# Performance work log

Hardware: AMD Instinct MI355X
Metric: run time of the kernel (lower is better)

Reference implementation:

```python
import jax, jax.numpy as jnp
import numpy as np

N = 4096       # graph nodes (= image batch)
FIN = 2048     # resnet50 feature dim
HD = 256       # hidden_dim
C = 10         # num_classes
THRESH = 0.05  # cosine-sim threshold for adjacency
ATTN_SLOPE = 0.2   # DGL GATConv leaky-relu slope
MLP_SLOPE = 0.01   # F.leaky_relu default slope


def setup_inputs() -> dict:
    key = jax.random.key(0)
    ks = jax.random.split(key, 24)
    g = lambda k, shp, s=0.05: (jax.random.normal(k, shp, jnp.float32) * s)
    inp = {
        "x": jax.random.normal(ks[0], (N, FIN), jnp.float32),
        # GAT layer 1: 2048 -> 256, 4 heads, linear residual
        "W0": g(ks[1], (FIN, 4 * HD)),
        "al0": g(ks[2], (4, HD)), "ar0": g(ks[3], (4, HD)),
        "b0": jnp.zeros((4 * HD,), jnp.float32),
        "R0": g(ks[4], (FIN, 4 * HD)),
        # GAT mid layer: 256 -> 256, 4 heads, linear residual
        "W1": g(ks[5], (HD, 4 * HD)),
        "al1": g(ks[6], (4, HD)), "ar1": g(ks[7], (4, HD)),
        "b1": jnp.zeros((4 * HD,), jnp.float32),
        "R1": g(ks[8], (HD, 4 * HD)),
        # GAT final layer: 256 -> 256, 1 head, identity residual
        "W2": g(ks[9], (HD, HD)),
        "al2": g(ks[10], (1, HD)), "ar2": g(ks[11], (1, HD)),
        "b2": jnp.zeros((HD,), jnp.float32),
        # heads
        "Wl1": g(ks[12], (FIN + HD, 1024)), "bl1": jnp.zeros((1024,), jnp.float32),
        "Wc1": g(ks[13], (1024, C)), "bc1": jnp.zeros((C,), jnp.float32),
        "Wc2": g(ks[14], (FIN, C)), "bc2": jnp.zeros((C,), jnp.float32),
    }
    return inp


def _gat(h, mask, W, al, ar, b, R):
    """DGL GATConv with residual=True, masked dense edge-softmax.
    h: [N, Fin]; mask: [N, N] bool (mask[dst, src]); returns [N, H, Fout]."""
    n = h.shape[0]
    H, F = al.shape
    feat = (h @ W).reshape(n, H, F)                      # [N, H, F] src/dst projections
    el = jnp.einsum('nhf,hf->nh', feat, al)              # src score
    er = jnp.einsum('nhf,hf->nh', feat, ar)              # dst score
    e = er[:, None, :] + el[None, :, :]                  # [dst, src, H]
    e = jnp.where(e > 0, e, ATTN_SLOPE * e)              # leaky relu
    e = jnp.where(mask[:, :, None], e, -jnp.inf)
    alpha = jax.nn.softmax(e, axis=1)                    # edge softmax over src
    rst = jnp.einsum('dsh,shf->dhf', alpha, feat)        # aggregate
    res = (h @ R).reshape(n, H, F) if R is not None else h.reshape(n, -1, F)
    return rst + res + b.reshape(1, H, F)


def reference(x, W0, al0, ar0, b0, R0, W1, al1, ar1, b1, R1,
              W2, al2, ar2, b2, Wl1, bl1, Wc1, bc1, Wc2, bc2):
    # dynamic threshold graph from cosine similarity
    xn = x / jnp.linalg.norm(x, axis=1, keepdims=True)
    mask = (xn @ xn.T) > THRESH                          # symmetric, includes self-loops
    # stacked GAT layers, heads summed
    h = jax.nn.relu(_gat(x, mask, W0, al0, ar0, b0, R0).sum(axis=1))
    h = jax.nn.relu(_gat(h, mask, W1, al1, ar1, b1, R1).sum(axis=1))
    h = _gat(h, mask, W2, al2, ar2, b2, None).sum(axis=1)  # last layer: no relu
    # MLP heads
    z = jnp.concatenate([x, h], axis=1)                  # [N, 2048+256]
    z = jax.nn.leaky_relu(z @ Wl1 + bl1, MLP_SLOPE)
    logits_1 = z @ Wc1 + bc1
    logits_2 = x @ Wc2 + bc2
    return logits_1, logits_2
```

## Files before the change

kernel.cpp:

```cpp
#include <hip/hip_runtime.h>
#include <cstdint>
#include <cstddef>

#define NNODE 4096
#define FIND  2048
#define HD_   256
#define NC_   10
#define THRESH_ 0.05f
#define LOG2E_ 1.4426950408889634f

typedef unsigned long long u64;
typedef __attribute__((ext_vector_type(8))) short bf16x8;
typedef __attribute__((ext_vector_type(4))) float f32x4;

__device__ inline unsigned short f2bf_rne(float f){
  unsigned u = __builtin_bit_cast(unsigned, f);
  unsigned r = u + 0x7FFFu + ((u >> 16) & 1u);
  return (unsigned short)(r >> 16);
}
__device__ inline float bf2f(unsigned short h){
  unsigned u = ((unsigned)h) << 16;
  return __builtin_bit_cast(float, u);
}
__device__ __forceinline__ float fexp2(float x){ return __builtin_amdgcn_exp2f(x); }

__device__ __forceinline__ void gld16(const void* g, void* l){
  __builtin_amdgcn_global_load_lds(
      (const __attribute__((address_space(1))) unsigned int*)g,
      (__attribute__((address_space(3))) unsigned int*)l, 16, 0, 0);
}

__global__ void rownorm_bf(const float* __restrict__ x,
                           unsigned short* __restrict__ oh, unsigned short* __restrict__ ol){
  int row = blockIdx.x; int t = threadIdx.x;
  const float4* xr = reinterpret_cast<const float4*>(x + (size_t)row*FIND);
  float s = 0.f;
  #pragma unroll
  for (int i = 0; i < FIND/4/256; ++i){
    float4 v = xr[t + i*256];
    s += v.x*v.x + v.y*v.y + v.z*v.z + v.w*v.w;
  }
  #pragma unroll
  for (int o = 32; o > 0; o >>= 1) s += __shfl_down(s, o);
  __shared__ float red[4];
  __shared__ float invn;
  if ((t & 63) == 0) red[t >> 6] = s;
  __syncthreads();
  if (t == 0) invn = rsqrtf(red[0] + red[1] + red[2] + red[3]);
  __syncthreads();
  float inv = invn;
  #pragma unroll
  for (int i = 0; i < FIND/4/256; ++i){
    float4 v = xr[t + i*256];
    float a[4] = {v.x*inv, v.y*inv, v.z*inv, v.w*inv};
    ushort4 hv, lv;
    unsigned short* hp = &hv.x; unsigned short* lp = &lv.x;
    #pragma unroll
    for (int j = 0; j < 4; ++j){
      unsigned short h = f2bf_rne(a[j]);
      hp[j] = h; lp[j] = f2bf_rne(a[j] - bf2f(h));
    }
    size_t off = (size_t)row*FIND + (t + i*256)*4;
    *reinterpret_cast<ushort4*>(oh + off) = hv;
    *reinterpret_cast<ushort4*>(ol + off) = lv;
  }
}

__global__ void f2bf1_k(const float* __restrict__ in, unsigned short* __restrict__ oh, int n4){
  int idx = blockIdx.x*256 + threadIdx.x;
  if (idx >= n4) return;
  float4 v = reinterpret_cast<const float4*>(in)[idx];
  ushort4 hv;
  hv.x = f2bf_rne(v.x); hv.y = f2bf_rne(v.y);
  hv.z = f2bf_rne(v.z); hv.w = f2bf_rne(v.w);
  reinterpret_cast<ushort4*>(oh)[idx] = hv;
}

template<int H>
__global__ void foldT_k(const float* __restrict__ R, unsigned short* __restrict__ oh,
                        unsigned short* __restrict__ ol, int K, int F, int ktiles){
  int bid = blockIdx.x;
  int f0 = (bid / ktiles) * 64, k0 = (bid % ktiles) * 64;
  __shared__ float tile[64][65];
  int t = threadIdx.x;
  {
    int tf = t & 63, tk4 = t >> 6;
    #pragma unroll
    for (int m = 0; m < 16; ++m){
      int kl = tk4 + m*4;
      float s = 0.f;
      #pragma unroll
      for (int h = 0; h < H; ++h)
        s += R[(size_t)(k0 + kl)*(H*F) + h*F + f0 + tf];
      tile[kl][tf] = s;
    }
  }
  __syncthreads();
  {
    int tk = t & 63, tf4 = t >> 6;
    #pragma unroll
    for (int m = 0; m < 16; ++m){
      int fl = tf4 + m*4;
      float s = tile[tk][fl];
      unsigned short hv = f2bf_rne(s);
      size_t o = (size_t)(f0 + fl)*K + k0 + tk;
      oh[o] = hv;
      ol[o] = f2bf_rne(s - bf2f(hv));
    }
  }
}

__global__ void bfold_k(const float* __restrict__ b, float* __restrict__ out, int H, int F){
  int f = threadIdx.x;
  if (f < F){
    float s = 0.f;
    for (int h = 0; h < H; ++h) s += b[h*F + f];
    out[f] = s;
  }
}

__global__ void mega_gemm(const unsigned short* __restrict__ XNh, const unsigned short* __restrict__ XNl,
                          const unsigned short* __restrict__ Xh,
                          const unsigned short* __restrict__ W0h, const unsigned short* __restrict__ W0l,
                          const unsigned short* __restrict__ WLh, const unsigned short* __restrict__ WLl,
                          float* __restrict__ FT, unsigned short* __restrict__ FTB,
                          float* __restrict__ Z1, u64* __restrict__ Mk){
  __shared__ unsigned short smem[4*128*32];
  unsigned short* sAh = smem;
  unsigned short* sAl = smem + 4096;
  unsigned short* sBh = smem + 8192;
  unsigned short* sBl = smem + 12288;
  const int t = threadIdx.x, lane = t & 63, w = t >> 6;
  const int wr = w >> 1, wc = w & 1, l15 = lane & 15, lg = lane >> 4;

  const int bid = blockIdx.x;
  const int xcd = bid & 7, idx = bid >> 3;

  int role, brow, bcol;
  const unsigned short *Ah, *Al = nullptr, *Bh, *Bl;
  float* C = nullptr; int ldc = 0; size_t ldb;
  if (idx < 66){
    role = 0;
    int g = xcd*66 + idx;
    int rem = g, i = 0;
    while (rem >= 32 - i){ rem -= 32 - i; ++i; }
    brow = i; bcol = i + rem;
    Ah = XNh; Al = XNl; Bh = XNh; Bl = XNl; ldb = FIND;
  } else if (idx < 106){
    role = 1;
    int l = xcd*40 + (idx - 66);
    brow = l / 10; bcol = l % 10;
    Ah = Xh; Bh = W0h; Bl = W0l; ldb = FIND;
    C = FT; ldc = 1280;
  } else {
    role = 2;
    int l = xcd*32 + (idx - 106);
    brow = l >> 3; bcol = l & 7;
    Ah = Xh; Bh = WLh; Bl = WLl; ldb = 2304;
    C = Z1; ldc = 1024;
  }
  const bool three = (role == 0);
  const int row0 = brow*128, col0 = bcol*128;

  const int c0 = 2*w, c1 = 2*w + 1;
  const int rsub = lane >> 2, piece = lane & 3;
  const size_t ld2a = (size_t)FIND*2, ld2b = ldb*2;
  const size_t a0 = (size_t)(row0 + 16*c0 + rsub)*ld2a + piece*16;
  const size_t a1 = (size_t)(row0 + 16*c1 + rsub)*ld2a + piece*16;
  const size_t b0 = (size_t)(col0 + 16*c0 + rsub)*ld2b + piece*16;
  const size_t b1 = (size_t)(col0 + 16*c1 + rsub)*ld2b + piece*16;
  const char* pA0h = (const char*)Ah + a0;  const char* pA1h = (const char*)Ah + a1;
  const char* pA0l = three ? (const char*)Al + a0 : nullptr;
  const char* pA1l = three ? (const char*)Al + a1 : nullptr;
  const char* pB0h = (const char*)Bh + b0;  const char* pB1h = (const char*)Bh + b1;
  const char* pB0l = (const char*)Bl + b0;  const char* pB1l = (const char*)Bl + b1;
  char* lA0h = (char*)sAh + c0*1024;  char* lA1h = (char*)sAh + c1*1024;
  char* lA0l = (char*)sAl + c0*1024;  char* lA1l = (char*)sAl + c1*1024;
  char* lB0h = (char*)sBh + c0*1024;  char* lB1h = (char*)sBh + c1*1024;
  char* lB0l = (char*)sBl + c0*1024;  char* lB1l = (char*)sBl + c1*1024;

  f32x4 acc[4][4] = {};
  for (int kt = 0; kt < 64; ++kt){
    __syncthreads();
    gld16(pA0h, lA0h); gld16(pA1h, lA1h);
    if (three){
      gld16(pA0l, lA0l); gld16(pA1l, lA1l);
      pA0l += 64; pA1l += 64;
    }
    gld16(pB0h, lB0h); gld16(pB1h, lB1h);
    gld16(pB0l, lB0l); gld16(pB1l, lB1l);
    pA0h += 64; pA1h += 64;
    pB0h += 64; pB1h += 64; pB0l += 64; pB1l += 64;
    __syncthreads();
    bf16x8 fb_h[4], fb_l[4];
    #pragma unroll
    for (int j = 0; j < 4; ++j){
      int bo = (wc*64 + j*16 + l15)*32 + lg*8;
      fb_h[j] = *reinterpret_cast<const bf16x8*>(sBh + bo);
      fb_l[j] = *reinterpret_cast<const bf16x8*>(sBl + bo);
    }
    #pragma unroll
    for (int i = 0; i < 4; ++i){
      int ao = (wr*64 + i*16 + l15)*32 + lg*8;
      bf16x8 fah = *reinterpret_cast<const bf16x8*>(sAh + ao);
      #pragma unroll
      for (int j = 0; j < 4; ++j){
        acc[i][j] = __builtin_amdgcn_mfma_f32_16x16x32_bf16(fah, fb_h[j], acc[i][j], 0, 0, 0);
        acc[i][j] = __builtin_amdgcn_mfma_f32_16x16x32_bf16(fah, fb_l[j], acc[i][j], 0, 0, 0);
      }
      if (three){
        bf16x8 fal = *reinterpret_cast<const bf16x8*>(sAl + ao);
        #pragma unroll
        for (int j = 0; j < 4; ++j)
          acc[i][j] = __builtin_amdgcn_mfma_f32_16x16x32_bf16(fal, fb_h[j], acc[i][j], 0, 0, 0);
      }
    }
  }

  if (role == 0){
    #pragma unroll
    for (int i = 0; i < 4; ++i){
      #pragma unroll
      for (int r = 0; r < 4; ++r){
        u64 bits = 0ull;
        #pragma unroll
        for (int j = 0; j < 4; ++j)
          if (acc[i][j][r] > THRESH_) bits |= 1ull << (j*16 + l15);
        #pragma unroll
        for (int m = 1; m <= 8; m <<= 1) bits |= __shfl_xor(bits, m);
        if (l15 == 0){
          int gr = row0 + wr*64 + i*16 + lg*4 + r;
          Mk[(size_t)gr*64 + (col0 >> 6) + wc] = bits;
        }
      }
    }
    if (row0 != col0){
      #pragma unroll
      for (int j = 0; j < 4; ++j){
        u64 tb = 0ull;
        #pragma unroll
        for (int i = 0; i < 4; ++i)
          #pragma unroll
          for (int r = 0; r < 4; ++r)
            if (acc[i][j][r] > THRESH_) tb |= 1ull << (i*16 + lg*4 + r);
        tb |= __shfl_xor(tb, 16);
        tb |= __shfl_xor(tb, 32);
        if (lg == 0){
          int gc = col0 + wc*64 + j*16 + l15;
          Mk[(size_t)gc*64 + (row0 >> 6) + wr] = tb;
        }
      }
    }
  } else {
    const int f32min = (role == 1) ? 1024 : 0;
    #pragma unroll
    for (int i = 0; i < 4; ++i){
      int gr = row0 + wr*64 + i*16 + lg*4;
      #pragma unroll
      for (int j = 0; j < 4; ++j){
        int gc = col0 + wc*64 + j*16 + l15;
        #pragma unroll
        for (int r = 0; r < 4; ++r){
          float v = acc[i][j][r];
          if (role == 1) FTB[(size_t)(gr + r)*1280 + gc] = f2bf_rne(v);
          if (gc >= f32min) C[(size_t)(gr + r)*ldc + gc] = v;
        }
      }
    }
  }
}

template<int EPI>
__global__ void gemm_bf(const unsigned short* __restrict__ Ah,
                        const unsigned short* __restrict__ Bh, const unsigned short* __restrict__ Bl,
                        float* __restrict__ C, unsigned short* __restrict__ Cb,
                        int K, int lda, int ldb, int ldc, int gridx,
                        const float* __restrict__ bias, float param, int f32min){
  __shared__ unsigned short smem[3*128*32];
  unsigned short* sAh = smem;
  unsigned short* sBh = smem + 4096;
  unsigned short* sBl = smem + 8192;
  const int t = threadIdx.x, lane = t & 63, w = t >> 6;
  const int wr = w >> 1, wc = w & 1, l15 = lane & 15, lg = lane >> 4;

  int nwg = gridDim.x, bid = blockIdx.x;
  int wg = ((nwg & 7) == 0) ? ((bid & 7)*(nwg >> 3) + (bid >> 3)) : bid;
  int brow = wg / gridx, bcol = wg % gridx;
  const int row0 = brow*128, col0 = bcol*128;

  const int c0 = 2*w, c1 = 2*w + 1;
  const int rsub = lane >> 2, piece = lane & 3;
  const size_t ld2a = (size_t)lda*2, ld2b = (size_t)ldb*2;
  const size_t a0 = (size_t)(row0 + 16*c0 + rsub)*ld2a + piece*16;
  const size_t a1 = (size_t)(row0 + 16*c1 + rsub)*ld2a + piece*16;
  const size_t b0 = (size_t)(col0 + 16*c0 + rsub)*ld2b + piece*16;
  const size_t b1 = (size_t)(col0 + 16*c1 + rsub)*ld2b + piece*16;
  const char* pA0h = (const char*)Ah + a0;  const char* pA1h = (const char*)Ah + a1;
  const char* pB0h = (const char*)Bh + b0;  const char* pB1h = (const char*)Bh + b1;
  const char* pB0l = (const char*)Bl + b0;  const char* pB1l = (const char*)Bl + b1;
  char* lA0h = (char*)sAh + c0*1024;  char* lA1h = (char*)sAh + c1*1024;
  char* lB0h = (char*)sBh + c0*1024;  char* lB1h = (char*)sBh + c1*1024;
  char* lB0l = (char*)sBl + c0*1024;  char* lB1l = (char*)sBl + c1*1024;

  f32x4 acc[4][4] = {};
  const int nk = K >> 5;
  for (int kt = 0; kt < nk; ++kt){
    __syncthreads();
    gld16(pA0h, lA0h); gld16(pA1h, lA1h);
    gld16(pB0h, lB0h); gld16(pB1h, lB1h);
    gld16(pB0l, lB0l); gld16(pB1l, lB1l);
    pA0h += 64; pA1h += 64;
    pB0h += 64; pB1h += 64; pB0l += 64; pB1l += 64;
    __syncthreads();
    bf16x8 fb_h[4], fb_l[4];
    #pragma unroll
    for (int j = 0; j < 4; ++j){
      int bo = (wc*64 + j*16 + l15)*32 + lg*8;
      fb_h[j] = *reinterpret_cast<const bf16x8*>(sBh + bo);
      fb_l[j] = *reinterpret_cast<const bf16x8*>(sBl + bo);
    }
    #pragma unroll
    for (int i = 0; i < 4; ++i){
      int ao = (wr*64 + i*16 + l15)*32 + lg*8;
      bf16x8 fah = *reinterpret_cast<const bf16x8*>(sAh + ao);
      #pragma unroll
      for (int j = 0; j < 4; ++j){
        acc[i][j] = __builtin_amdgcn_mfma_f32_16x16x32_bf16(fah, fb_h[j], acc[i][j], 0, 0, 0);
        acc[i][j] = __builtin_amdgcn_mfma_f32_16x16x32_bf16(fah, fb_l[j], acc[i][j], 0, 0, 0);
      }
    }
  }

  #pragma unroll
  for (int i = 0; i < 4; ++i){
    int gr = row0 + wr*64 + i*16 + lg*4;
    #pragma unroll
    for (int j = 0; j < 4; ++j){
      int gc = col0 + wc*64 + j*16 + l15;
      #pragma unroll
      for (int r = 0; r < 4; ++r){
        float v = acc[i][j][r];
        size_t o = (size_t)(gr + r)*ldc + gc;
        if (EPI == 3){
          v += C[o] + bias[gc];
          v = v > 0.f ? v : param*v;
          C[o] = v;
        } else {
          if (Cb) Cb[o] = f2bf_rne(v);
          if (gc >= f32min) C[o] = v;
        }
      }
    }
  }
}

template<int H>
__global__ void el_er_k(const unsigned short* __restrict__ feat, int ldf,
                        const float* __restrict__ al, const float* __restrict__ ar,
                        float* __restrict__ el2, float* __restrict__ er2){
  int n = blockIdx.x, t = threadIdx.x;
  __shared__ float red[8];
  #pragma unroll
  for (int h = 0; h < H; ++h){
    float v = bf2f(feat[(size_t)n*ldf + h*HD_ + t]);
    float a = v * al[h*HD_ + t];
    float b = v * ar[h*HD_ + t];
    #pragma unroll
    for (int o = 32; o > 0; o >>= 1){ a += __shfl_down(a, o); b += __shfl_down(b, o); }
    if ((t & 63) == 0){ red[t >> 6] = a; red[4 + (t >> 6)] = b; }
    __syncthreads();
    if (t == 0){
      el2[n*H + h] = (red[0] + red[1] + red[2] + red[3]) * LOG2E_;
      er2[n*H + h] = (red[4] + red[5] + red[6] + red[7]) * LOG2E_;
    }
    __syncthreads();
  }
}

template<int H>
__global__ void elmax_k(const float* __restrict__ el2, float* __restrict__ out){
  int h = blockIdx.x, t = threadIdx.x;
  float m = -1e30f;
  for (int n = t; n < NNODE; n += 256) m = fmaxf(m, el2[(size_t)n*H + h]);
  #pragma unroll
  for (int o = 32; o > 0; o >>= 1) m = fmaxf(m, __shfl_down(m, o));
  __shared__ float red[4];
  if ((t & 63) == 0) red[t >> 6] = m;
  __syncthreads();
  if (t == 0) out[h] = fmaxf(fmaxf(red[0], red[1]), fmaxf(red[2], red[3]));
}

template<int H, bool RELU, bool OUTF32>
__global__ void sagg_k(const unsigned short* __restrict__ FTB, int ldf,
                       const u64* __restrict__ Mk,
                       const float* __restrict__ el2, const float* __restrict__ er2,
                       const float* __restrict__ melg2,
                       const float* __restrict__ res, int ldres,
                       const float* __restrict__ bias,
                       float* __restrict__ outf,
                       unsigned short* __restrict__ oh){
  int d = blockIdx.x, t = threadIdx.x;
  const int g = t >> 6, q = t & 63;
  const int h = (H == 4) ? g : 0;
  const int wlo = (H == 1) ? g*16 : 0;
  const int whi = (H == 1) ? wlo + 16 : 64;
  const float er2d = er2[(size_t)d*H + h];
  const float sub = er2d + melg2[h];
  const float m2 = fmaxf(sub, 0.2f*sub);
  const unsigned short* fb = FTB + 4*q + ((H == 4) ? 256*g : 0);
  float4 acc = {0.f, 0.f, 0.f, 0.f};
  float sm = 0.f;
  for (int wdi = wlo; wdi < whi; ++wdi){
    u64 bits = Mk[(size_t)d*64 + wdi];
    while (bits){
      int b = __builtin_ctzll(bits);
      bits &= bits - 1ull;
      int s = wdi*64 + b;
      float sc = er2d + el2[(size_t)s*H + h];
      sc = fmaxf(sc, 0.2f*sc);
      float wt = fexp2(sc - m2);
      sm += wt;
      ushort4 v = *reinterpret_cast<const ushort4*>(fb + (size_t)s*ldf);
      acc.x += wt*bf2f(v.x); acc.y += wt*bf2f(v.y);
      acc.z += wt*bf2f(v.z); acc.w += wt*bf2f(v.w);
    }
  }
  __shared__ float lred[4][256];
  __shared__ float lsm[4];
  if (H == 4){
    float inv = 1.f / sm;
    acc.x *= inv; acc.y *= inv; acc.z *= inv; acc.w *= inv;
  } else if (q == 0){
    lsm[g] = sm;
  }
  lred[g][q*4+0] = acc.x; lred[g][q*4+1] = acc.y;
  lred[g][q*4+2] = acc.z; lred[g][q*4+3] = acc.w;
  __syncthreads();
  float v = ((lred[0][t] + lred[1][t]) + lred[2][t]) + lred[3][t];
  if (H == 1) v /= (lsm[0] + lsm[1]) + (lsm[2] + lsm[3]);
  v += res[(size_t)d*ldres + t] + bias[t];
  if (RELU) v = fmaxf(v, 0.f);
  if (OUTF32) outf[(size_t)d*HD_ + t] = v;
  oh[(size_t)d*HD_ + t] = f2bf_rne(v);
}

__global__ void head_k(const float* __restrict__ A, int K, const float* __restrict__ W,
                       const float* __restrict__ b, float* __restrict__ out){
  int row = blockIdx.x, t = threadIdx.x;
  float p[NC_];
  #pragma unroll
  for (int j = 0; j < NC_; ++j) p[j] = 0.f;
  for (int k = t; k < K; k += 256){
    float a = A[(size_t)row*K + k];
    #pragma unroll
    for (int j = 0; j < NC_; ++j) p[j] += a * W[k*NC_ + j];
  }
  #pragma unroll
  for (int j = 0; j < NC_; ++j){
    #pragma unroll
    for (int o = 32; o > 0; o >>= 1) p[j] += __shfl_down(p[j], o);
  }
  __shared__ float red[4][NC_];
  if ((t & 63) == 0){
    #pragma unroll
    for (int j = 0; j < NC_; ++j) red[t >> 6][j] = p[j];
  }
  __syncthreads();
  if (t < NC_)
    out[(size_t)row*NC_ + t] = red[0][t] + red[1][t] + red[2][t] + red[3][t] + b[t];
}

extern "C" void kernel_launch(void* const* d_in, const int* in_sizes, int n_in,
                              void* d_out, int out_size, void* d_ws, size_t ws_size,
                              hipStream_t stream){
  const float* x   = (const float*)d_in[0];
  const float* W0  = (const float*)d_in[1];
  const float* al0 = (const float*)d_in[2];
  const float* ar0 = (const float*)d_in[3];
  const float* b0  = (const float*)d_in[4];
  const float* R0  = (const float*)d_in[5];
  const float* W1  = (const float*)d_in[6];
  const float* al1 = (const float*)d_in[7];
  const float* ar1 = (const float*)d_in[8];
  const float* b1  = (const float*)d_in[9];
  const float* R1  = (const float*)d_in[10];
  const float* W2  = (const float*)d_in[11];
  const float* al2 = (const float*)d_in[12];
  const float* ar2 = (const float*)d_in[13];
  const float* b2  = (const float*)d_in[14];
  const float* Wl1 = (const float*)d_in[15];
  const float* bl1 = (const float*)d_in[16];
  const float* Wc1 = (const float*)d_in[17];
  const float* bc1 = (const float*)d_in[18];
  const float* Wc2 = (const float*)d_in[19];
  const float* bc2 = (const float*)d_in[20];
  (void)in_sizes; (void)n_in; (void)out_size; (void)ws_size;

  char* ws = (char*)d_ws;
  size_t off = 0;
  auto alloc = [&](size_t bytes)->char*{
    char* p = ws + off; off += (bytes + 255) & ~(size_t)255; return p;
  };
  typedef unsigned short us;
  u64* MASK = (u64*)alloc((size_t)NNODE*64*8);
  us* W0h = (us*)alloc((size_t)1280*2048*2);  us* W0l = (us*)alloc((size_t)1280*2048*2);
  us* W1h = (us*)alloc((size_t)1280*256*2);   us* W1l = (us*)alloc((size_t)1280*256*2);
  us* W2h = (us*)alloc((size_t)256*256*2);    us* W2l = (us*)alloc((size_t)256*256*2);
  us* WLh = (us*)alloc((size_t)1024*2304*2);  us* WLl = (us*)alloc((size_t)1024*2304*2);
  float* BF0 = (float*)alloc(256*4);
  float* BF1 = (float*)alloc(256*4);
  float* EL2 = (float*)alloc((size_t)NNODE*4*4);
  float* ER2 = (float*)alloc((size_t)NNODE*4*4);
  float* MELG = (float*)alloc(4*4);
  us* XNh = (us*)alloc((size_t)NNODE*FIND*2);
  us* XNl = (us*)alloc((size_t)NNODE*FIND*2);
  us* Xh  = (us*)alloc((size_t)NNODE*FIND*2);
  float* FT = (float*)alloc((size_t)NNODE*1280*4);
  us* FTB = (us*)alloc((size_t)NNODE*1280*2);
  float* H2 = (float*)alloc((size_t)NNODE*HD_*4);
  us* H1h = (us*)alloc((size_t)NNODE*HD_*2);
  us* H2h = (us*)alloc((size_t)NNODE*HD_*2);
  us* H3h = (us*)alloc((size_t)NNODE*HD_*2);
  float* Z1 = (float*)alloc((size_t)NNODE*1024*4);

  float* out1 = (float*)d_out;
  float* out2 = out1 + (size_t)NNODE*NC_;

  foldT_k<1><<<512, 256, 0, stream>>>(W0, W0h, W0l, 2048, 1024, 32);
  foldT_k<4><<<128, 256, 0, stream>>>(R0, W0h + (size_t)1024*2048, W0l + (size_t)1024*2048, 2048, 256, 32);
  foldT_k<1><<< 64, 256, 0, stream>>>(W1, W1h, W1l, 256, 1024, 4);
  foldT_k<4><<< 16, 256, 0, stream>>>(R1, W1h + (size_t)1024*256, W1l + (size_t)1024*256, 256, 256, 4);
  foldT_k<1><<< 16, 256, 0, stream>>>(W2, W2h, W2l, 256, 256, 4);
  foldT_k<1><<<576, 256, 0, stream>>>(Wl1, WLh, WLl, 2304, 1024, 36);
  bfold_k<<<1, 256, 0, stream>>>(b0, BF0, 4, 256);
  bfold_k<<<1, 256, 0, stream>>>(b1, BF1, 4, 256);
  f2bf1_k<<<(NNODE*FIND/4+255)/256, 256, 0, stream>>>(x, Xh, NNODE*FIND/4);
  rownorm_bf<<<NNODE, 256, 0, stream>>>(x, XNh, XNl);

  mega_gemm<<<1104, 256, 0, stream>>>(XNh, XNl, Xh, W0h, W0l, WLh, WLl, FT, FTB, Z1, MASK);

  el_er_k<4><<<NNODE, 256, 0, stream>>>(FTB, 1280, al0, ar0, EL2, ER2);
  elmax_k<4><<<4, 256, 0, stream>>>(EL2, MELG);
  sagg_k<4,true,false><<<NNODE, 256, 0, stream>>>(FTB, 1280, MASK, EL2, ER2, MELG,
      FT + 1024, 1280, BF0, nullptr, H1h);

  gemm_bf<0><<<320, 256, 0, stream>>>(H1h, W1h, W1l, FT, FTB,
      256, 256, 256, 1280, 10, nullptr, 0.f, 1024);
  el_er_k<4><<<NNODE, 256, 0, stream>>>(FTB, 1280, al1, ar1, EL2, ER2);
  elmax_k<4><<<4, 256, 0, stream>>>(EL2, MELG);
  sagg_k<4,true,true><<<NNODE, 256, 0, stream>>>(FTB, 1280, MASK, EL2, ER2, MELG,
      FT + 1024, 1280, BF1, H2, H2h);

  gemm_bf<0><<<64, 256, 0, stream>>>(H2h, W2h, W2l, FT, FTB,
      256, 256, 256, 256, 2, nullptr, 0.f, 1 << 30);
  el_er_k<1><<<NNODE, 256, 0, stream>>>(FTB, 256, al2, ar2, EL2, ER2);
  elmax_k<1><<<1, 256, 0, stream>>>(EL2, MELG);
  sagg_k<1,false,false><<<NNODE, 256, 0, stream>>>(FTB, 256, MASK, EL2, ER2, MELG,
      H2, 256, b2, nullptr, H3h);

  gemm_bf<3><<<256, 256, 0, stream>>>(H3h, WLh + 2048, WLl + 2048, Z1, nullptr,
      256, 256, 2304, 1024, 8, bl1, 0.01f, 0);

  head_k<<<NNODE, 256, 0, stream>>>(Z1, 1024, Wc1, bc1, out1);
  head_k<<<NNODE, 256, 0, stream>>>(x, FIND, Wc2, bc2, out2);
}
```

Baseline: 536.6 us.

## Fold attention vectors into weights and fuse score computation into aggregation

Precomputes W·al and W·ar per head so the src and dst attention scores become small GEMVs on the layer input instead of reductions over projected features. Layer-0 scores are computed from x in fp32 by a new GEMV kernel, and scores for the next layer are produced in the epilogue of each aggregation kernel. The per-head max is tracked with an atomicMax on order-preserving encoded floats. This removes the separate el_er and elmax launches and drops bf16 writes of the residual columns, at the cost of extra prep kernels and atomics, with slightly different rounding since scores now come from fp32 inputs rather than bf16 features.

```diff
diff --git a/kernel.cpp b/kernel.cpp
--- a/kernel.cpp
+++ b/kernel.cpp
@@ -23,6 +23,15 @@
   return __builtin_bit_cast(float, u);
 }
 __device__ __forceinline__ float fexp2(float x){ return __builtin_amdgcn_exp2f(x); }
+
+__device__ inline unsigned fenc(float f){
+  unsigned u = __builtin_bit_cast(unsigned, f);
+  return (u & 0x80000000u) ? ~u : (u | 0x80000000u);
+}
+__device__ inline float fdec(unsigned k){
+  unsigned u = (k & 0x80000000u) ? (k & 0x7FFFFFFFu) : ~k;
+  return __builtin_bit_cast(float, u);
+}
 
 __device__ __forceinline__ void gld16(const void* g, void* l){
   __builtin_amdgcn_global_load_lds(
@@ -116,6 +125,60 @@
     float s = 0.f;
     for (int h = 0; h < H; ++h) s += b[h*F + f];
     out[f] = s;
+  }
+}
+
+template<int H, bool INIT>
+__global__ void valprep_k(const float* __restrict__ W, const float* __restrict__ al,
+                          const float* __restrict__ ar, float* __restrict__ val,
+                          unsigned* __restrict__ melg){
+  int t = threadIdx.x, lane = t & 63, w = t >> 6;
+  if (INIT && blockIdx.x == 0 && t < 12) melg[t] = 0u;
+  int task = blockIdx.x*4 + w;
+  int k = task / H, h = task % H;
+  float4 wv = *reinterpret_cast<const float4*>(W + (size_t)k*(H*256) + h*256 + lane*4);
+  float4 av = *reinterpret_cast<const float4*>(al + h*256 + lane*4);
+  float4 rv = *reinterpret_cast<const float4*>(ar + h*256 + lane*4);
+  float e = wv.x*av.x + wv.y*av.y + wv.z*av.z + wv.w*av.w;
+  float r = wv.x*rv.x + wv.y*rv.y + wv.z*rv.z + wv.w*rv.w;
+  #pragma unroll
+  for (int o = 32; o > 0; o >>= 1){ e += __shfl_down(e, o); r += __shfl_down(r, o); }
+  if (lane == 0){
+    val[(size_t)k*2*H + h] = e;
+    val[(size_t)k*2*H + H + h] = r;
+  }
+}
+
+__global__ void el0gemv_k(const float* __restrict__ x, const float* __restrict__ val0,
+                          float* __restrict__ el2, float* __restrict__ er2,
+                          unsigned* __restrict__ melg0){
+  int n = blockIdx.x, t = threadIdx.x;
+  float acc[8] = {};
+  #pragma unroll
+  for (int i = 0; i < 8; ++i){
+    int k = i*256 + t;
+    float xv = x[(size_t)n*FIND + k];
+    float4 v0 = *reinterpret_cast<const float4*>(val0 + (size_t)k*8);
+    float4 v1 = *reinterpret_cast<const float4*>(val0 + (size_t)k*8 + 4);
+    acc[0] += xv*v0.x; acc[1] += xv*v0.y; acc[2] += xv*v0.z; acc[3] += xv*v0.w;
+    acc[4] += xv*v1.x; acc[5] += xv*v1.y; acc[6] += xv*v1.z; acc[7] += xv*v1.w;
+  }
+  __shared__ float red[4][8];
+  #pragma unroll
+  for (int j = 0; j < 8; ++j){
+    float v = acc[j];
+    #pragma unroll
+    for (int o = 32; o > 0; o >>= 1) v += __shfl_down(v, o);
+    if ((t & 63) == 0) red[t >> 6][j] = v;
+  }
+  __syncthreads();
+  if (t < 4){
+    int h = t;
+    float el = (red[0][h] + red[1][h] + red[2][h] + red[3][h]) * LOG2E_;
+    float er = (red[0][4+h] + red[1][4+h] + red[2][4+h] + red[3][4+h]) * LOG2E_;
+    el2[(size_t)n*4 + h] = el;
+    er2[(size_t)n*4 + h] = er;
+    atomicMax(&melg0[h], fenc(el));
   }
 }
 
@@ -262,7 +325,7 @@
         #pragma unroll
         for (int r = 0; r < 4; ++r){
           float v = acc[i][j][r];
-          if (role == 1) FTB[(size_t)(gr + r)*1280 + gc] = f2bf_rne(v);
+          if (role == 1 && gc < 1024) FTB[(size_t)(gr + r)*1280 + gc] = f2bf_rne(v);
           if (gc >= f32min) C[(size_t)(gr + r)*ldc + gc] = v;
         }
       }
@@ -275,7 +338,7 @@
                         const unsigned short* __restrict__ Bh, const unsigned short* __restrict__ Bl,
                         float* __restrict__ C, unsigned short* __restrict__ Cb,
                         int K, int lda, int ldb, int ldc, int gridx,
-                        const float* __restrict__ bias, float param, int f32min){
+                        const float* __restrict__ bias, float param, int f32min, int bfmax){
   __shared__ unsigned short smem[3*128*32];
   unsigned short* sAh = smem;
   unsigned short* sBh = smem + 4096;
@@ -346,7 +409,7 @@
           v = v > 0.f ? v : param*v;
           C[o] = v;
         } else {
-          if (Cb) Cb[o] = f2bf_rne(v);
+          if (gc < bfmax) Cb[o] = f2bf_rne(v);
           if (gc >= f32min) C[o] = v;
         }
       }
@@ -354,58 +417,25 @@
   }
 }
 
-template<int H>
-__global__ void el_er_k(const unsigned short* __restrict__ feat, int ldf,
-                        const float* __restrict__ al, const float* __restrict__ ar,
-                        float* __restrict__ el2, float* __restrict__ er2){
-  int n = blockIdx.x, t = threadIdx.x;
-  __shared__ float red[8];
-  #pragma unroll
-  for (int h = 0; h < H; ++h){
-    float v = bf2f(feat[(size_t)n*ldf + h*HD_ + t]);
-    float a = v * al[h*HD_ + t];
-    float b = v * ar[h*HD_ + t];
-    #pragma unroll
-    for (int o = 32; o > 0; o >>= 1){ a += __shfl_down(a, o); b += __shfl_down(b, o); }
-    if ((t & 63) == 0){ red[t >> 6] = a; red[4 + (t >> 6)] = b; }
-    __syncthreads();
-    if (t == 0){
-      el2[n*H + h] = (red[0] + red[1] + red[2] + red[3]) * LOG2E_;
-      er2[n*H + h] = (red[4] + red[5] + red[6] + red[7]) * LOG2E_;
-    }
-    __syncthreads();
-  }
-}
-
-template<int H>
-__global__ void elmax_k(const float* __restrict__ el2, float* __restrict__ out){
-  int h = blockIdx.x, t = threadIdx.x;
-  float m = -1e30f;
-  for (int n = t; n < NNODE; n += 256) m = fmaxf(m, el2[(size_t)n*H + h]);
-  #pragma unroll
-  for (int o = 32; o > 0; o >>= 1) m = fmaxf(m, __shfl_down(m, o));
-  __shared__ float red[4];
-  if ((t & 63) == 0) red[t >> 6] = m;
-  __syncthreads();
-  if (t == 0) out[h] = fmaxf(fmaxf(red[0], red[1]), fmaxf(red[2], red[3]));
-}
-
-template<int H, bool RELU, bool OUTF32>
+template<int H, bool RELU, bool OUTF32, int NEXTJ>
 __global__ void sagg_k(const unsigned short* __restrict__ FTB, int ldf,
                        const u64* __restrict__ Mk,
                        const float* __restrict__ el2, const float* __restrict__ er2,
-                       const float* __restrict__ melg2,
+                       const unsigned* __restrict__ melg,
                        const float* __restrict__ res, int ldres,
                        const float* __restrict__ bias,
                        float* __restrict__ outf,
-                       unsigned short* __restrict__ oh){
+                       unsigned short* __restrict__ oh,
+                       const float* __restrict__ valw,
+                       float* __restrict__ el2n, float* __restrict__ er2n,
+                       unsigned* __restrict__ melgn){
   int d = blockIdx.x, t = threadIdx.x;
   const int g = t >> 6, q = t & 63;
   const int h = (H == 4) ? g : 0;
   const int wlo = (H == 1) ? g*16 : 0;
   const int whi = (H == 1) ? wlo + 16 : 64;
   const float er2d = er2[(size_t)d*H + h];
-  const float sub = er2d + melg2[h];
+  const float sub = er2d + fdec(melg[h]);
   const float m2 = fmaxf(sub, 0.2f*sub);
   const unsigned short* fb = FTB + 4*q + ((H == 4) ? 256*g : 0);
   float4 acc = {0.f, 0.f, 0.f, 0.f};
@@ -442,6 +472,37 @@
   if (RELU) v = fmaxf(v, 0.f);
   if (OUTF32) outf[(size_t)d*HD_ + t] = v;
   oh[(size_t)d*HD_ + t] = f2bf_rne(v);
+
+  if (NEXTJ > 0){
+    float p[NEXTJ > 0 ? NEXTJ : 1];
+    if (NEXTJ == 8){
+      float4 w0 = *reinterpret_cast<const float4*>(valw + (size_t)t*8);
+      float4 w1 = *reinterpret_cast<const float4*>(valw + (size_t)t*8 + 4);
+      p[0] = v*w0.x; p[1] = v*w0.y; p[2] = v*w0.z; p[3] = v*w0.w;
+      p[4] = v*w1.x; p[5] = v*w1.y; p[6] = v*w1.z; p[7] = v*w1.w;
+    } else if (NEXTJ == 2){
+      float2 w0 = *reinterpret_cast<const float2*>(valw + (size_t)t*2);
+      p[0] = v*w0.x; p[1] = v*w0.y;
+    }
+    __shared__ float ered[4][NEXTJ > 0 ? NEXTJ : 1];
+    #pragma unroll
+    for (int j = 0; j < NEXTJ; ++j){
+      float pv = p[j];
+      #pragma unroll
+      for (int o = 32; o > 0; o >>= 1) pv += __shfl_down(pv, o);
+      if (q == 0) ered[g][j] = pv;
+    }
+    __syncthreads();
+    const int NH = NEXTJ/2;
+    if (t < NH){
+      int hh = t;
+      float el = (ered[0][hh] + ered[1][hh] + ered[2][hh] + ered[3][hh]) * LOG2E_;
+      float er = (ered[0][NH+hh] + ered[1][NH+hh] + ered[2][NH+hh] + ered[3][NH+hh]) * LOG2E_;
+      el2n[(size_t)d*NH + hh] = el;
+      er2n[(size_t)d*NH + hh] = er;
+      atomicMax(&melgn[hh], fenc(el));
+    }
+  }
 }
 
 __global__ void head_k(const float* __restrict__ A, int K, const float* __restrict__ W,
@@ -509,9 +570,16 @@
   us* WLh = (us*)alloc((size_t)1024*2304*2);  us* WLl = (us*)alloc((size_t)1024*2304*2);
   float* BF0 = (float*)alloc(256*4);
   float* BF1 = (float*)alloc(256*4);
-  float* EL2 = (float*)alloc((size_t)NNODE*4*4);
-  float* ER2 = (float*)alloc((size_t)NNODE*4*4);
-  float* MELG = (float*)alloc(4*4);
+  float* VAL0 = (float*)alloc((size_t)2048*8*4);
+  float* VALW1 = (float*)alloc((size_t)256*8*4);
+  float* VALW2 = (float*)alloc((size_t)256*2*4);
+  float* EL0 = (float*)alloc((size_t)NNODE*4*4);
+  float* ER0 = (float*)alloc((size_t)NNODE*4*4);
+  float* EL1 = (float*)alloc((size_t)NNODE*4*4);
+  float* ER1 = (float*)alloc((size_t)NNODE*4*4);
+  float* EL2c = (float*)alloc((size_t)NNODE*4);
+  float* ER2c = (float*)alloc((size_t)NNODE*4);
+  unsigned* MELG = (unsigned*)alloc(12*4);
   us* XNh = (us*)alloc((size_t)NNODE*FIND*2);
   us* XNl = (us*)alloc((size_t)NNODE*FIND*2);
   us* Xh  = (us*)alloc((size_t)NNODE*FIND*2);
@@ -536,30 +604,28 @@
   bfold_k<<<1, 256, 0, stream>>>(b1, BF1, 4, 256);
   f2bf1_k<<<(NNODE*FIND/4+255)/256, 256, 0, stream>>>(x, Xh, NNODE*FIND/4);
   rownorm_bf<<<NNODE, 256, 0, stream>>>(x, XNh, XNl);
+  valprep_k<4,true ><<<2048, 256, 0, stream>>>(W0, al0, ar0, VAL0, MELG);
+  valprep_k<4,false><<< 256, 256, 0, stream>>>(W1, al1, ar1, VALW1, MELG);
+  valprep_k<1,false><<<  64, 256, 0, stream>>>(W2, al2, ar2, VALW2, MELG);
+  el0gemv_k<<<NNODE, 256, 0, stream>>>(x, VAL0, EL0, ER0, MELG);
 
   mega_gemm<<<1104, 256, 0, stream>>>(XNh, XNl, Xh, W0h, W0l, WLh, WLl, FT, FTB, Z1, MASK);
 
-  el_er_k<4><<<NNODE, 256, 0, stream>>>(FTB, 1280, al0, ar0, EL2, ER2);
-  elmax_k<4><<<4, 256, 0, stream>>>(EL2, MELG);
-  sagg_k<4,true,false><<<NNODE, 256, 0, stream>>>(FTB, 1280, MASK, EL2, ER2, MELG,
-      FT + 1024, 1280, BF0, nullptr, H1h);
+  sagg_k<4,true,false,8><<<NNODE, 256, 0, stream>>>(FTB, 1280, MASK, EL0, ER0, MELG,
+      FT + 1024, 1280, BF0, nullptr, H1h, VALW1, EL1, ER1, MELG + 4);
 
   gemm_bf<0><<<320, 256, 0, stream>>>(H1h, W1h, W1l, FT, FTB,
-      256, 256, 256, 1280, 10, nullptr, 0.f, 1024);
-  el_er_k<4><<<NNODE, 256, 0, stream>>>(FTB, 1280, al1, ar1, EL2, ER2);
-  elmax_k<4><<<4, 256, 0, stream>>>(EL2, MELG);
-  sagg_k<4,true,true><<<NNODE, 256, 0, stream>>>(FTB, 1280, MASK, EL2, ER2, MELG,
-      FT + 1024, 1280, BF1, H2, H2h);
+      256, 256, 256, 1280, 10, nullptr, 0.f, 1024, 1024);
+  sagg_k<4,true,true,2><<<NNODE, 256, 0, stream>>>(FTB, 1280, MASK, EL1, ER1, MELG + 4,
+      FT + 1024, 1280, BF1, H2, H2h, VALW2, EL2c, ER2c, MELG + 8);
 
   gemm_bf<0><<<64, 256, 0, stream>>>(H2h, W2h, W2l, FT, FTB,
-      256, 256, 256, 256, 2, nullptr, 0.f, 1 << 30);
-  el_er_k<1><<<NNODE, 256, 0, stream>>>(FTB, 256, al2, ar2, EL2, ER2);
-  elmax_k<1><<<1, 256, 0, stream>>>(EL2, MELG);
-  sagg_k<1,false,false><<<NNODE, 256, 0, stream>>>(FTB, 256, MASK, EL2, ER2, MELG,
-      H2, 256, b2, nullptr, H3h);
+      256, 256, 256, 256, 2, nullptr, 0.f, 1 << 30, 1 << 30);
+  sagg_k<1,false,false,0><<<NNODE, 256, 0, stream>>>(FTB, 256, MASK, EL2c, ER2c, MELG + 8,
+      H2, 256, b2, nullptr, H3h, nullptr, nullptr, nullptr, nullptr);
 
   gemm_bf<3><<<256, 256, 0, stream>>>(H3h, WLh + 2048, WLl + 2048, Z1, nullptr,
-      256, 256, 2304, 1024, 8, bl1, 0.01f, 0);
+      256, 256, 2304, 1024, 8, bl1, 0.01f, 0, 0);
 
   head_k<<<NNODE, 256, 0, stream>>>(Z1, 1024, Wc1, bc1, out1);
   head_k<<<NNODE, 256, 0, stream>>>(x, FIND, Wc2, bc2, out2);
```

Measured after the change: 739.1 us. 37.7% more time.
